# Performance work log

Measured on AMD Instinct MI355X. Metric: run time of the kernel, lower is better.

The kernel has to match this reference:

```python
import jax, jax.numpy as jnp
import numpy as np

B, S = 1024, 512
V, E, H, T = 50000, 300, 800, 50


def setup_inputs() -> dict:
    key = jax.random.key(0)
    ks = jax.random.split(key, 8)
    ids = jax.random.randint(ks[0], (B, S), 0, V, dtype=jnp.int64 if jax.config.jax_enable_x64 else jnp.int32)
    return {
        "ids": ids,
        "rho": jax.random.normal(ks[1], (V, E), jnp.float32) * 0.02,
        "alpha": jax.random.normal(ks[2], (T, E), jnp.float32) * 0.02,
        "W1": jax.random.normal(ks[3], (E, H), jnp.float32) * 0.05,
        "b1": jnp.zeros((H,), jnp.float32),
        "Wmu": jax.random.normal(ks[4], (H, T), jnp.float32) * 0.05,
        "bmu": jnp.zeros((T,), jnp.float32),
        "Wlv": jax.random.normal(ks[5], (H, T), jnp.float32) * 0.05,
        "blv": jnp.zeros((T,), jnp.float32),
    }


def reference(ids, rho, alpha, W1, b1, Wmu, bmu, Wlv, blv):
    b, s = ids.shape
    v = rho.shape[0]
    # bag-of-words histogram: scatter-add instead of dense one_hot+reduce_sum
    bows = jnp.zeros((b, v), rho.dtype).at[jnp.arange(b)[:, None], ids].add(1.0)
    # zero out special tokens 1 and 2 (original: x * (1 - sum(one_hot([1,2]))))
    bows = bows.at[:, jnp.array([1, 2])].set(0.0)
    normal_bows = bows / jnp.sum(bows, axis=-1, keepdims=True)
    # encoder (eval mode: dropout is identity)
    x = jnp.einsum('bv,ve->be', normal_bows, rho)
    h = jax.nn.relu(x @ W1 + b1)
    mu_theta = h @ Wmu + bmu
    logsigma_theta = h @ Wlv + blv
    kl_theta = -0.5 * jnp.sum(1.0 + logsigma_theta - mu_theta**2 - jnp.exp(logsigma_theta), axis=-1)
    # reparameterize (eval/inference mode): z = mu
    theta = jax.nn.softmax(mu_theta, axis=-1)  # [B, T]
    beta = jax.nn.softmax(jnp.einsum('te,ve->tv', alpha, rho), axis=-1)  # [T, V]
    lookup = jnp.log(theta @ beta + 1e-5)  # [B, V]
    recon_loss = -jnp.sum(lookup * bows, axis=-1)
    loss = jnp.mean(recon_loss) + jnp.mean(kl_theta)
    return theta, loss
```

## Files before the change

kernel.cpp:

```cpp
#include <hip/hip_runtime.h>
#include <math.h>


#define Bn 1024
#define Sn 512
#define Vn 50000
#define En 300
#define Hn 800
#define Tn 50
#define KP 320
#define BSTR 64
#define W1FRAG_N (50 * 10 * 64 * 8)
#define WFRAG_N  (8 * 25 * 64 * 8)
#define NRANGE 8
#define VRANGE (Vn / NRANGE)
#define CASTB (Vn * (KP / 4) / 256)
#define K4B (Vn / 16)

typedef __bf16 bf16x8 __attribute__((ext_vector_type(8)));
typedef float  f32x4  __attribute__((ext_vector_type(4)));

__device__ __forceinline__ float waveReduceSum(float v) {
    #pragma unroll
    for (int off = 32; off > 0; off >>= 1) v += __shfl_xor(v, off, 64);
    return v;
}
__device__ __forceinline__ float waveReduceMax(float v) {
    #pragma unroll
    for (int off = 32; off > 0; off >>= 1) v = fmaxf(v, __shfl_xor(v, off, 64));
    return v;
}
__device__ __forceinline__ unsigned short f2bf(float x) {
    unsigned u = __float_as_uint(x);
    return (unsigned short)((u + 0x7FFFu + ((u >> 16) & 1u)) >> 16);
}
__device__ __forceinline__ float bf_lo(unsigned u) { return __uint_as_float(u << 16); }
__device__ __forceinline__ float bf_hi(unsigned u) { return __uint_as_float(u & 0xFFFF0000u); }
__device__ __forceinline__ int lane_prefix(unsigned long long m) {
    return __builtin_amdgcn_mbcnt_hi((unsigned)(m >> 32),
           __builtin_amdgcn_mbcnt_lo((unsigned)m, 0));
}

#define ACC8(u) { a0 += bf_lo((u).x); a1 += bf_hi((u).x); \
                  a2 += bf_lo((u).y); a3 += bf_hi((u).y); \
                  a4 += bf_lo((u).z); a5 += bf_hi((u).z); \
                  a6 += bf_lo((u).w); a7 += bf_hi((u).w); }

__global__ __launch_bounds__(256) void ka_init(
        const float4* __restrict__ rho4, ushort4* __restrict__ rhoh4,
        const float* __restrict__ alpha, const float* __restrict__ W1,
        const float* __restrict__ Wmu, const float* __restrict__ Wlv,
        unsigned short* __restrict__ bfrag, unsigned short* __restrict__ w1frag,
        unsigned short* __restrict__ wfrag, float* __restrict__ topicsumR,
        float* __restrict__ loss) {
    if (blockIdx.x < CASTB) {
        const int i = blockIdx.x * 256 + threadIdx.x;
        int v = i / (KP / 4), s = i - v * (KP / 4);
        ushort4 p = {0, 0, 0, 0};
        if (s < En / 4) {
            float4 r = rho4[v * (En / 4) + s];
            p.x = f2bf(r.x); p.y = f2bf(r.y); p.z = f2bf(r.z); p.w = f2bf(r.w);
        }
        rhoh4[i] = p;
        return;
    }
    const int gid = (blockIdx.x - CASTB) * 256 + threadIdx.x;
    if (gid < 512) topicsumR[gid] = 0.f;
    if (gid == 520) *loss = 0.f;
    if (gid < 4 * 10 * 64 * 8) {
        int j = gid & 7;
        int lane = (gid >> 3) & 63;
        int rest = gid >> 9;
        int kt = rest % 10, w = rest / 10;
        int t = 16 * w + (lane & 15);
        int e = kt * 32 + (lane >> 4) * 8 + j;
        bfrag[gid] = (t < Tn && e < En) ? f2bf(alpha[t * En + e]) : (unsigned short)0;
    }
    if (gid < W1FRAG_N) {
        int j = gid & 7, lane = (gid >> 3) & 63, rest = gid >> 9;
        int kt = rest % 10, nt = rest / 10;
        int e = kt * 32 + (lane >> 4) * 8 + j;
        int hcol = nt * 16 + (lane & 15);
        w1frag[gid] = (e < En) ? f2bf(W1[e * Hn + hcol]) : (unsigned short)0;
    } else {
        int g2 = gid - W1FRAG_N;
        if (g2 < WFRAG_N) {
            int j = g2 & 7, lane = (g2 >> 3) & 63, rest = g2 >> 9;
            int kt = rest % 25, nt = rest / 25;
            int k = kt * 32 + (lane >> 4) * 8 + j;
            int t = (nt & 3) * 16 + (lane & 15);
            float val = 0.f;
            if (t < Tn) val = (nt < 4) ? Wmu[k * Tn + t] : Wlv[k * Tn + t];
            wfrag[g2] = f2bf(val);
        }
    }
}

__global__ __launch_bounds__(256) void kb_beta_tokens(
        const unsigned short* __restrict__ rhoh,
        const unsigned short* __restrict__ bfrag,
        unsigned int* __restrict__ betaU32, float* __restrict__ topicsumR,
        const int* __restrict__ ids, int* __restrict__ toks,
        int* __restrict__ cnt, float* __restrict__ xbarP) {
    __shared__ unsigned short trans[16 * 66];
    __shared__ __align__(16) int sid[Sn];
    __shared__ int sfid[Sn];
    __shared__ float xred[4][320];
    __shared__ int scount, sfull;
    const int tid = threadIdx.x;
    const int wave = tid >> 6, lane = tid & 63;

    if (blockIdx.x < K4B) {
        const int quad = lane >> 4, l15 = lane & 15;
        const int v0 = blockIdx.x * 16;
        const unsigned short* arow = rhoh + (size_t)(v0 + l15) * KP + quad * 8;
        f32x4 acc = {0.f, 0.f, 0.f, 0.f};
        #pragma unroll
        for (int kt = 0; kt < 10; ++kt) {
            bf16x8 a = *(const bf16x8*)(arow + kt * 32);
            bf16x8 bv = *(const bf16x8*)(bfrag + ((wave * 10 + kt) * 64 + lane) * 8);
            acc = __builtin_amdgcn_mfma_f32_16x16x32_bf16(a, bv, acc, 0, 0, 0);
        }
        float ts = 0.f;
        #pragma unroll
        for (int r = 0; r < 4; ++r) {
            float ev = expf(acc[r]);
            ts += ev;
            trans[(quad * 4 + r) * 66 + 16 * wave + l15] = f2bf(ev);
        }
        ts += __shfl_xor(ts, 16, 64);
        ts += __shfl_xor(ts, 32, 64);
        const int t = 16 * wave + l15;
        if (lane < 16 && t < Tn)
            atomicAdd(&topicsumR[(blockIdx.x & 7) * 64 + t], ts);
        __syncthreads();
        unsigned int* dst = betaU32 + (size_t)v0 * 32;
        const unsigned int* tr32 = (const unsigned int*)trans;
        for (int i = tid; i < 16 * 32; i += 256)
            dst[i] = tr32[(i >> 5) * 33 + (i & 31)];
        return;
    }
    const int blk = blockIdx.x - K4B;
    const int r = blk & (NRANGE - 1), b = blk >> 3;
    const int lo = r * VRANGE, hi = lo + VRANGE;
    if (tid == 0) { scount = 0; sfull = 0; }
    __syncthreads();
    #pragma unroll
    for (int s0 = 0; s0 < Sn; s0 += 256) {
        int id = ids[b * Sn + s0 + tid];
        bool val = (id != 1 && id != 2);
        bool inr = val && id >= lo && id < hi;
        unsigned long long mb = __ballot(inr);
        int pre = lane_prefix(mb);
        int wc = __popcll(mb);
        int base = 0;
        if (lane == 0 && wc) base = atomicAdd(&scount, wc);
        base = __shfl(base, 0, 64);
        if (inr) sid[base + pre] = id;
        if (r == 0) {
            unsigned long long fb = __ballot(val);
            int fpre = lane_prefix(fb);
            int fwc = __popcll(fb);
            int fbase = 0;
            if (lane == 0 && fwc) fbase = atomicAdd(&sfull, fwc);
            fbase = __shfl(fbase, 0, 64);
            if (val) sfid[fbase + fpre] = id;
        }
    }
    __syncthreads();
    if (r == 0) {
        const int nf = sfull;
        for (int i = tid; i < nf; i += 256) toks[b * Sn + i] = sfid[i];
        if (tid == 0) cnt[b] = nf;
    }
    const int m = scount;
    float a0 = 0.f, a1 = 0.f, a2 = 0.f, a3 = 0.f;
    float a4 = 0.f, a5 = 0.f, a6 = 0.f, a7 = 0.f;
    if (lane < 40) {
        const uint4* rb = (const uint4*)rhoh;
        int s = wave;
        for (; s + 12 < m; s += 16) {
            int i0 = sid[s], i1 = sid[s + 4], i2 = sid[s + 8], i3 = sid[s + 12];
            uint4 u0 = rb[(size_t)i0 * 40 + lane];
            uint4 u1 = rb[(size_t)i1 * 40 + lane];
            uint4 u2 = rb[(size_t)i2 * 40 + lane];
            uint4 u3 = rb[(size_t)i3 * 40 + lane];
            ACC8(u0); ACC8(u1); ACC8(u2); ACC8(u3);
        }
        for (; s < m; s += 4) {
            uint4 u = rb[(size_t)sid[s] * 40 + lane];
            ACC8(u);
        }
        float* xw = &xred[wave][lane * 8];
        xw[0] = a0; xw[1] = a1; xw[2] = a2; xw[3] = a3;
        xw[4] = a4; xw[5] = a5; xw[6] = a6; xw[7] = a7;
    }
    __syncthreads();
    float* xbp = xbarP + ((size_t)b * NRANGE + r) * KP;
    for (int c = tid; c < KP; c += 256)
        xbp[c] = xred[0][c] + xred[1][c] + xred[2][c] + xred[3][c];
}

__global__ __launch_bounds__(256) void k2m_h(
        const float* __restrict__ xbarP, const int* __restrict__ cnt,
        const unsigned short* __restrict__ w1frag,
        const float* __restrict__ b1, unsigned short* __restrict__ hbh) {
    __shared__ unsigned short xs[16 * 328];
    __shared__ float invn[16];
    const int tid = threadIdx.x;
    const int wave = tid >> 6, lane = tid & 63;
    const int quad = lane >> 4, l15 = lane & 15;
    const int b0 = blockIdx.x * 16;
    if (tid < 16) invn[tid] = 1.0f / (float)cnt[b0 + tid];
    __syncthreads();
    for (int i = tid; i < 16 * (KP / 4); i += 256) {
        int row = i / (KP / 4), e4 = (i - row * (KP / 4)) * 4;
        const float* bp = xbarP + ((size_t)(b0 + row) * NRANGE) * KP + e4;
        float sx = 0.f, sy = 0.f, sz = 0.f, sw_ = 0.f;
        #pragma unroll
        for (int rr = 0; rr < NRANGE; ++rr) {
            float4 v = *(const float4*)(bp + rr * KP);
            sx += v.x; sy += v.y; sz += v.z; sw_ += v.w;
        }
        float in = invn[row];
        ushort4 o;
        o.x = f2bf(sx * in); o.y = f2bf(sy * in);
        o.z = f2bf(sz * in); o.w = f2bf(sw_ * in);
        *(ushort4*)&xs[row * 328 + e4] = o;
    }
    __syncthreads();
    const int nt = blockIdx.y * 4 + wave;
    if (nt < 50) {
        const unsigned short* arow = xs + l15 * 328 + quad * 8;
        f32x4 acc = {0.f, 0.f, 0.f, 0.f};
        #pragma unroll
        for (int kt = 0; kt < 10; ++kt) {
            bf16x8 a = *(const bf16x8*)(arow + kt * 32);
            bf16x8 bv = *(const bf16x8*)(w1frag + ((size_t)(nt * 10 + kt) * 64 + lane) * 8);
            acc = __builtin_amdgcn_mfma_f32_16x16x32_bf16(a, bv, acc, 0, 0, 0);
        }
        const int col = nt * 16 + l15;
        const float bias = b1[col];
        #pragma unroll
        for (int r = 0; r < 4; ++r) {
            int row = b0 + quad * 4 + r;
            hbh[(size_t)row * Hn + col] = f2bf(fmaxf(acc[r] + bias, 0.f));
        }
    }
}

__global__ __launch_bounds__(256) void k3_theta(
        const unsigned short* __restrict__ hbh,
        const unsigned short* __restrict__ wfrag,
        const float* __restrict__ bmu, const float* __restrict__ blv,
        float* __restrict__ theta, float* __restrict__ loss) {
    __shared__ float mlds[16 * 65];
    __shared__ float llds[16 * 65];
    const int tid = threadIdx.x;
    const int wave = tid >> 6, lane = tid & 63;
    const int quad = lane >> 4, l15 = lane & 15;
    const int b0 = blockIdx.x * 16;
    const unsigned short* arow = hbh + (size_t)(b0 + l15) * Hn + quad * 8;
    f32x4 am = {0.f, 0.f, 0.f, 0.f}, al = {0.f, 0.f, 0.f, 0.f};
    #pragma unroll
    for (int kt = 0; kt < 25; ++kt) {
        bf16x8 a  = *(const bf16x8*)(arow + kt * 32);
        bf16x8 bm = *(const bf16x8*)(wfrag + ((size_t)(wave * 25 + kt) * 64 + lane) * 8);
        bf16x8 bl = *(const bf16x8*)(wfrag + ((size_t)((4 + wave) * 25 + kt) * 64 + lane) * 8);
        am = __builtin_amdgcn_mfma_f32_16x16x32_bf16(a, bm, am, 0, 0, 0);
        al = __builtin_amdgcn_mfma_f32_16x16x32_bf16(a, bl, al, 0, 0, 0);
    }
    const int t = wave * 16 + l15;
    const float bm_ = (t < Tn) ? bmu[t] : 0.f;
    const float bl_ = (t < Tn) ? blv[t] : 0.f;
    #pragma unroll
    for (int r = 0; r < 4; ++r) {
        int row = quad * 4 + r;
        mlds[row * 65 + t] = am[r] + bm_;
        llds[row * 65 + t] = al[r] + bl_;
    }
    __syncthreads();
    const int tt = (lane < Tn) ? lane : (Tn - 1);
    const bool act = (lane < Tn);
    float klacc = 0.f;
    #pragma unroll
    for (int k = 0; k < 4; ++k) {
        int row = wave * 4 + k;
        float mu = mlds[row * 65 + tt];
        float lv = llds[row * 65 + tt];
        float m = waveReduceMax(act ? mu : -1e30f);
        float ex = act ? expf(mu - m) : 0.f;
        float ssum = waveReduceSum(ex);
        if (act) theta[(b0 + row) * Tn + lane] = ex / ssum;
        klacc += waveReduceSum(act ? (1.f + lv - mu * mu - expf(lv)) : 0.f);
    }
    if (lane == 0) atomicAdd(loss, -0.5f * klacc * (1.0f / (float)Bn));
}

__global__ __launch_bounds__(256) void k6_recon(
        const int* __restrict__ toks, const int* __restrict__ cnt,
        const float* __restrict__ theta, const float* __restrict__ topicsumR,
        const unsigned short* __restrict__ betaUh, float* __restrict__ loss) {
    __shared__ float sw[Tn];
    __shared__ float swred[4];
    const int b = blockIdx.x, tid = threadIdx.x;
    if (tid < Tn) {
        float z = 0.f;
        #pragma unroll
        for (int j = 0; j < 8; ++j) z += topicsumR[j * 64 + tid];
        sw[tid] = theta[b * Tn + tid] / z;
    }
    __syncthreads();
    float wr[Tn];
    #pragma unroll
    for (int t = 0; t < Tn; ++t) wr[t] = sw[t];
    float lsum = 0.f;
    const int n = cnt[b];
    for (int i = tid; i < n; i += 256) {
        int v = toks[b * Sn + i];
        const uint4* q = (const uint4*)(betaUh + (size_t)v * BSTR);
        float dot = 0.f;
        #pragma unroll
        for (int k = 0; k < 6; ++k) {
            uint4 u = q[k];
            int t = 8 * k;
            dot += wr[t]     * bf_lo(u.x) + wr[t + 1] * bf_hi(u.x);
            dot += wr[t + 2] * bf_lo(u.y) + wr[t + 3] * bf_hi(u.y);
            dot += wr[t + 4] * bf_lo(u.z) + wr[t + 5] * bf_hi(u.z);
            dot += wr[t + 6] * bf_lo(u.w) + wr[t + 7] * bf_hi(u.w);
        }
        unsigned d = ((const unsigned*)q)[24];
        dot += wr[48] * bf_lo(d) + wr[49] * bf_hi(d);
        lsum += logf(dot + 1e-5f);
    }
    float s = waveReduceSum(lsum);
    const int wave = tid >> 6, lane = tid & 63;
    if (lane == 0) swred[wave] = s;
    __syncthreads();
    if (tid == 0) {
        float tot = swred[0] + swred[1] + swred[2] + swred[3];
        atomicAdd(loss, -tot * (1.0f / (float)Bn));
    }
}

extern "C" void kernel_launch(void* const* d_in, const int* in_sizes, int n_in,
                              void* d_out, int out_size, void* d_ws, size_t ws_size,
                              hipStream_t stream) {
    const int*   ids   = (const int*)d_in[0];
    const float* rho   = (const float*)d_in[1];
    const float* alpha = (const float*)d_in[2];
    const float* W1    = (const float*)d_in[3];
    const float* b1    = (const float*)d_in[4];
    const float* Wmu   = (const float*)d_in[5];
    const float* bmu   = (const float*)d_in[6];
    const float* Wlv   = (const float*)d_in[7];
    const float* blv   = (const float*)d_in[8];

    float* theta = (float*)d_out;
    float* loss  = theta + Bn * Tn;

    char* w = (char*)d_ws;
    float* topicsumR = (float*)w;               w += 8 * 64 * 4;
    unsigned short* bfrag = (unsigned short*)w; w += 4 * 10 * 64 * 8 * 2;
    unsigned short* w1frag = (unsigned short*)w; w += (size_t)W1FRAG_N * 2;
    unsigned short* wfrag = (unsigned short*)w;  w += (size_t)WFRAG_N * 2;
    int*   cnt      = (int*)w;                  w += Bn * 4;
    int*   toks     = (int*)w;                  w += Bn * Sn * 4;
    float* xbarP    = (float*)w;                w += (size_t)Bn * NRANGE * KP * 4;
    unsigned short* hbh = (unsigned short*)w;   w += (size_t)Bn * Hn * 2;
    unsigned short* rhoh = (unsigned short*)w;  w += (size_t)Vn * KP * 2;
    unsigned int* betaU32 = (unsigned int*)w;   w += (size_t)Vn * 128;

    const int k0grid = (W1FRAG_N + WFRAG_N + 255) / 256;
    ka_init<<<CASTB + k0grid, 256, 0, stream>>>(
        (const float4*)rho, (ushort4*)rhoh, alpha, W1, Wmu, Wlv,
        bfrag, w1frag, wfrag, topicsumR, loss);
    kb_beta_tokens<<<K4B + Bn * NRANGE, 256, 0, stream>>>(
        rhoh, bfrag, betaU32, topicsumR, ids, toks, cnt, xbarP);
    k2m_h<<<dim3(64, 13), 256, 0, stream>>>(xbarP, cnt, w1frag, b1, hbh);
    k3_theta<<<64, 256, 0, stream>>>(hbh, wfrag, bmu, blv, theta, loss);
    k6_recon<<<Bn, 256, 0, stream>>>(toks, cnt, theta, topicsumR,
                                     (const unsigned short*)betaU32, loss);
}
```

Before: 200.4 us.

## Double-buffer rho row gathers via global_load_lds and split normalization into own kernel

The per-bag embedding gather now assigns each wave a contiguous slice of tokens and streams rho rows into LDS with async global_load_lds, double-buffered in batches of four, accumulating with packed float2 adds. The goal is to overlap gather latency with accumulation. The bf16 cast of rho now writes 16-byte stores (8 elements per thread), which halves the cast grid. The xbarP reduction and normalization move out of k2m_h into a separate kx_norm kernel, so the 13 column-tile blocks no longer repeat it. This adds one kernel launch and an extra workspace buffer.

After: 208.1 us. 1.04x slower.

```diff
diff --git a/kernel.cpp b/kernel.cpp
--- a/kernel.cpp
+++ b/kernel.cpp
@@ -14,11 +14,12 @@
 #define WFRAG_N  (8 * 25 * 64 * 8)
 #define NRANGE 8
 #define VRANGE (Vn / NRANGE)
-#define CASTB (Vn * (KP / 4) / 256)
+#define CASTB 7813
 #define K4B (Vn / 16)
 
 typedef __bf16 bf16x8 __attribute__((ext_vector_type(8)));
 typedef float  f32x4  __attribute__((ext_vector_type(4)));
+typedef float  f32x2  __attribute__((ext_vector_type(2)));
 
 __device__ __forceinline__ float waveReduceSum(float v) {
     #pragma unroll
@@ -40,14 +41,20 @@
     return __builtin_amdgcn_mbcnt_hi((unsigned)(m >> 32),
            __builtin_amdgcn_mbcnt_lo((unsigned)m, 0));
 }
-
-#define ACC8(u) { a0 += bf_lo((u).x); a1 += bf_hi((u).x); \
-                  a2 += bf_lo((u).y); a3 += bf_hi((u).y); \
-                  a4 += bf_lo((u).z); a5 += bf_hi((u).z); \
-                  a6 += bf_lo((u).w); a7 += bf_hi((u).w); }
+__device__ __forceinline__ void gl_lds16(const void* g, void* l) {
+    __builtin_amdgcn_global_load_lds(
+        (const __attribute__((address_space(1))) void*)g,
+        (__attribute__((address_space(3))) void*)l, 16, 0, 0);
+}
+
+#define PKACC(u) { \
+    c0 += (f32x2){bf_lo((u).x), bf_hi((u).x)}; \
+    c1 += (f32x2){bf_lo((u).y), bf_hi((u).y)}; \
+    c2 += (f32x2){bf_lo((u).z), bf_hi((u).z)}; \
+    c3 += (f32x2){bf_lo((u).w), bf_hi((u).w)}; }
 
 __global__ __launch_bounds__(256) void ka_init(
-        const float4* __restrict__ rho4, ushort4* __restrict__ rhoh4,
+        const float4* __restrict__ rho4, unsigned short* __restrict__ rhoh,
         const float* __restrict__ alpha, const float* __restrict__ W1,
         const float* __restrict__ Wmu, const float* __restrict__ Wlv,
         unsigned short* __restrict__ bfrag, unsigned short* __restrict__ w1frag,
@@ -55,13 +62,25 @@
         float* __restrict__ loss) {
     if (blockIdx.x < CASTB) {
         const int i = blockIdx.x * 256 + threadIdx.x;
-        int v = i / (KP / 4), s = i - v * (KP / 4);
-        ushort4 p = {0, 0, 0, 0};
-        if (s < En / 4) {
-            float4 r = rho4[v * (En / 4) + s];
-            p.x = f2bf(r.x); p.y = f2bf(r.y); p.z = f2bf(r.z); p.w = f2bf(r.w);
-        }
-        rhoh4[i] = p;
+        if (i < Vn * (KP / 8)) {
+            int v = i / (KP / 8), s8 = i - v * (KP / 8);
+            int c = s8 * 8;
+            ushort4 o0 = {0, 0, 0, 0}, o1 = {0, 0, 0, 0};
+            if (c < En) {
+                float4 r = rho4[v * (En / 4) + s8 * 2];
+                o0.x = f2bf(r.x); o0.y = f2bf(r.y); o0.z = f2bf(r.z); o0.w = f2bf(r.w);
+            }
+            if (c + 4 < En) {
+                float4 r = rho4[v * (En / 4) + s8 * 2 + 1];
+                o1.x = f2bf(r.x); o1.y = f2bf(r.y); o1.z = f2bf(r.z); o1.w = f2bf(r.w);
+            }
+            uint4 st;
+            st.x = (unsigned)o0.x | ((unsigned)o0.y << 16);
+            st.y = (unsigned)o0.z | ((unsigned)o0.w << 16);
+            st.z = (unsigned)o1.x | ((unsigned)o1.y << 16);
+            st.w = (unsigned)o1.z | ((unsigned)o1.w << 16);
+            *(uint4*)(rhoh + (size_t)v * KP + c) = st;
+        }
         return;
     }
     const int gid = (blockIdx.x - CASTB) * 256 + threadIdx.x;
@@ -105,7 +124,8 @@
     __shared__ unsigned short trans[16 * 66];
     __shared__ __align__(16) int sid[Sn];
     __shared__ int sfid[Sn];
-    __shared__ float xred[4][320];
+    __shared__ __align__(16) float xred[4][320];
+    __shared__ __align__(16) char gbuf[4 * 2 * 4 * 640];
     __shared__ int scount, sfull;
     const int tid = threadIdx.x;
     const int wave = tid >> 6, lane = tid & 63;
@@ -174,26 +194,54 @@
         if (tid == 0) cnt[b] = nf;
     }
     const int m = scount;
-    float a0 = 0.f, a1 = 0.f, a2 = 0.f, a3 = 0.f;
-    float a4 = 0.f, a5 = 0.f, a6 = 0.f, a7 = 0.f;
+    const char* gb = (const char*)rhoh;
+    char* bufw = gbuf + wave * 5120;
+    f32x2 c0 = {0.f, 0.f}, c1 = {0.f, 0.f}, c2 = {0.f, 0.f}, c3 = {0.f, 0.f};
+    const int q = (m + 3) >> 2;
+    const int beg = min(wave * q, m);
+    const int end = min(beg + q, m);
+    const int nb = (end - beg + 3) >> 2;
+    const unsigned lo16 = (unsigned)lane * 16u;
+
+    #define GISSUE(S0, DST) { \
+        int r0 = sid[min((S0), end - 1)]; \
+        int r1 = sid[min((S0) + 1, end - 1)]; \
+        int r2 = sid[min((S0) + 2, end - 1)]; \
+        int r3 = sid[min((S0) + 3, end - 1)]; \
+        if (lane < 40) { \
+            gl_lds16(gb + (unsigned)r0 * 640u + lo16, (DST)); \
+            gl_lds16(gb + (unsigned)r1 * 640u + lo16, (DST) + 640); \
+            gl_lds16(gb + (unsigned)r2 * 640u + lo16, (DST) + 1280); \
+            gl_lds16(gb + (unsigned)r3 * 640u + lo16, (DST) + 1920); \
+        } }
+
+    if (nb > 0) {
+        GISSUE(beg, bufw);
+        for (int bch = 0; bch < nb; ++bch) {
+            const int cur = bch & 1;
+            if (bch + 1 < nb) {
+                GISSUE(beg + (bch + 1) * 4, bufw + ((cur ^ 1) * 2560));
+                asm volatile("s_waitcnt vmcnt(4)" ::: "memory");
+            } else {
+                asm volatile("s_waitcnt vmcnt(0)" ::: "memory");
+            }
+            __builtin_amdgcn_sched_barrier(0);
+            if (lane < 40) {
+                const char* bp = bufw + cur * 2560 + lane * 16;
+                const int rem = end - (beg + bch * 4);
+                uint4 u0 = *(const uint4*)(bp);
+                PKACC(u0);
+                if (rem > 1) { uint4 u = *(const uint4*)(bp + 640);  PKACC(u); }
+                if (rem > 2) { uint4 u = *(const uint4*)(bp + 1280); PKACC(u); }
+                if (rem > 3) { uint4 u = *(const uint4*)(bp + 1920); PKACC(u); }
+            }
+        }
+    }
+    #undef GISSUE
     if (lane < 40) {
-        const uint4* rb = (const uint4*)rhoh;
-        int s = wave;
-        for (; s + 12 < m; s += 16) {
-            int i0 = sid[s], i1 = sid[s + 4], i2 = sid[s + 8], i3 = sid[s + 12];
-            uint4 u0 = rb[(size_t)i0 * 40 + lane];
-            uint4 u1 = rb[(size_t)i1 * 40 + lane];
-            uint4 u2 = rb[(size_t)i2 * 40 + lane];
-            uint4 u3 = rb[(size_t)i3 * 40 + lane];
-            ACC8(u0); ACC8(u1); ACC8(u2); ACC8(u3);
-        }
-        for (; s < m; s += 4) {
-            uint4 u = rb[(size_t)sid[s] * 40 + lane];
-            ACC8(u);
-        }
         float* xw = &xred[wave][lane * 8];
-        xw[0] = a0; xw[1] = a1; xw[2] = a2; xw[3] = a3;
-        xw[4] = a4; xw[5] = a5; xw[6] = a6; xw[7] = a7;
+        *(float4*)(xw)     = (float4){c0[0], c0[1], c1[0], c1[1]};
+        *(float4*)(xw + 4) = (float4){c2[0], c2[1], c3[0], c3[1]};
     }
     __syncthreads();
     float* xbp = xbarP + ((size_t)b * NRANGE + r) * KP;
@@ -201,32 +249,37 @@
         xbp[c] = xred[0][c] + xred[1][c] + xred[2][c] + xred[3][c];
 }
 
+__global__ __launch_bounds__(256) void kx_norm(
+        const float* __restrict__ xbarP, const int* __restrict__ cnt,
+        unsigned short* __restrict__ xsg) {
+    const int i = blockIdx.x * 256 + threadIdx.x;
+    const int b = i / (KP / 4), e4 = (i - b * (KP / 4)) * 4;
+    const float in = 1.0f / (float)cnt[b];
+    const float* bp = xbarP + ((size_t)b * NRANGE) * KP + e4;
+    float sx = 0.f, sy = 0.f, sz = 0.f, sw_ = 0.f;
+    #pragma unroll
+    for (int rr = 0; rr < NRANGE; ++rr) {
+        float4 v = *(const float4*)(bp + rr * KP);
+        sx += v.x; sy += v.y; sz += v.z; sw_ += v.w;
+    }
+    ushort4 o;
+    o.x = f2bf(sx * in); o.y = f2bf(sy * in);
+    o.z = f2bf(sz * in); o.w = f2bf(sw_ * in);
+    *(ushort4*)&xsg[(size_t)b * KP + e4] = o;
+}
+
 __global__ __launch_bounds__(256) void k2m_h(
-        const float* __restrict__ xbarP, const int* __restrict__ cnt,
+        const unsigned short* __restrict__ xsg,
         const unsigned short* __restrict__ w1frag,
         const float* __restrict__ b1, unsigned short* __restrict__ hbh) {
     __shared__ unsigned short xs[16 * 328];
-    __shared__ float invn[16];
     const int tid = threadIdx.x;
     const int wave = tid >> 6, lane = tid & 63;
     const int quad = lane >> 4, l15 = lane & 15;
     const int b0 = blockIdx.x * 16;
-    if (tid < 16) invn[tid] = 1.0f / (float)cnt[b0 + tid];
-    __syncthreads();
-    for (int i = tid; i < 16 * (KP / 4); i += 256) {
-        int row = i / (KP / 4), e4 = (i - row * (KP / 4)) * 4;
-        const float* bp = xbarP + ((size_t)(b0 + row) * NRANGE) * KP + e4;
-        float sx = 0.f, sy = 0.f, sz = 0.f, sw_ = 0.f;
-        #pragma unroll
-        for (int rr = 0; rr < NRANGE; ++rr) {
-            float4 v = *(const float4*)(bp + rr * KP);
-            sx += v.x; sy += v.y; sz += v.z; sw_ += v.w;
-        }
-        float in = invn[row];
-        ushort4 o;
-        o.x = f2bf(sx * in); o.y = f2bf(sy * in);
-        o.z = f2bf(sz * in); o.w = f2bf(sw_ * in);
-        *(ushort4*)&xs[row * 328 + e4] = o;
+    for (int i = tid; i < 16 * (KP / 8); i += 256) {
+        int row = i / (KP / 8), e8 = (i - row * (KP / 8)) * 8;
+        *(uint4*)&xs[row * 328 + e8] = *(const uint4*)&xsg[(size_t)(b0 + row) * KP + e8];
     }
     __syncthreads();
     const int nt = blockIdx.y * 4 + wave;
@@ -370,14 +423,16 @@
     unsigned short* hbh = (unsigned short*)w;   w += (size_t)Bn * Hn * 2;
     unsigned short* rhoh = (unsigned short*)w;  w += (size_t)Vn * KP * 2;
     unsigned int* betaU32 = (unsigned int*)w;   w += (size_t)Vn * 128;
+    unsigned short* xsg = (unsigned short*)w;   w += (size_t)Bn * KP * 2;
 
     const int k0grid = (W1FRAG_N + WFRAG_N + 255) / 256;
     ka_init<<<CASTB + k0grid, 256, 0, stream>>>(
-        (const float4*)rho, (ushort4*)rhoh, alpha, W1, Wmu, Wlv,
+        (const float4*)rho, rhoh, alpha, W1, Wmu, Wlv,
         bfrag, w1frag, wfrag, topicsumR, loss);
     kb_beta_tokens<<<K4B + Bn * NRANGE, 256, 0, stream>>>(
         rhoh, bfrag, betaU32, topicsumR, ids, toks, cnt, xbarP);
-    k2m_h<<<dim3(64, 13), 256, 0, stream>>>(xbarP, cnt, w1frag, b1, hbh);
+    kx_norm<<<Bn * (KP / 4) / 256, 256, 0, stream>>>(xbarP, cnt, xsg);
+    k2m_h<<<dim3(64, 13), 256, 0, stream>>>(xsg, w1frag, b1, hbh);
     k3_theta<<<64, 256, 0, stream>>>(hbh, wfrag, bmu, blv, theta, loss);
     k6_recon<<<Bn, 256, 0, stream>>>(toks, cnt, theta, topicsumR,
                                      (const unsigned short*)betaU32, loss);
```
